# Kernel optimization log

Hardware: AMD Instinct MI355X
Metric: run time of the kernel (lower is better)

Reference implementation:

```python
import jax, jax.numpy as jnp
import numpy as np

ALPHA = 0.2  # LeakyReLU negative slope


def setup_inputs() -> dict:
    key = jax.random.key(0)
    k1, k2, k3, k4 = jax.random.split(key, 4)
    N, F_in, F_out = 8192, 512, 64
    x = jax.random.normal(k1, (N, F_in), dtype=jnp.float32)
    adj = jax.random.uniform(k2, (N, N), dtype=jnp.float32)
    W = jax.random.normal(k3, (F_in, F_out), dtype=jnp.float32) * 0.05
    a = jax.random.normal(k4, (2 * F_out, 1), dtype=jnp.float32) * 0.05
    return {"x": x, "adj": adj, "W": W, "a": a}


def reference(x, adj, W, a):
    F_out = W.shape[1]
    h = x @ W                                   # [N, F_out]
    # Additive attention decomposed: score[i,j] = h[i]·a1 + h[j]·a2
    # (equivalent to concat([h_i, h_j]) @ a, without the N×N×2F blowup)
    a1 = a[:F_out, 0]                           # [F_out]
    a2 = a[F_out:, 0]                           # [F_out]
    e = jax.nn.leaky_relu(h @ a1[:, None] + (h @ a2)[None, :], ALPHA)  # [N, N]
    attention = jax.nn.softmax(e * adj, axis=1)  # elementwise mult, as in source
    # dropout skipped (eval / training=False -> identity)
    h_prime = attention @ h                      # [N, F_out]
    return jax.nn.elu(h_prime)                   # concat=True branch
```

## Files before the change

kernel.cpp:

```cpp
#include <hip/hip_runtime.h>

#define ALPHA 0.2f

typedef __attribute__((ext_vector_type(2))) short short2v;
typedef __attribute__((ext_vector_type(8))) short short8v;
typedef __attribute__((ext_vector_type(4))) float f32x4;

__device__ __forceinline__ short f2bf(float f) {
  union { float f; unsigned u; } v; v.f = f;
  unsigned r = v.u + 0x7fffu + ((v.u >> 16) & 1u);
  return (short)(r >> 16);
}

__global__ __launch_bounds__(256) void k1_proj(
    const float* __restrict__ x, const float* __restrict__ W,
    const float* __restrict__ avec,
    short* __restrict__ hT, float* __restrict__ s1, float* __restrict__ s2) {
  __shared__ float xl[32 * 132];
  __shared__ float Wl[128 * 64];
  const int t   = threadIdx.x;
  const int rb  = blockIdx.x;
  const int row = t >> 3;
  const int fg  = t & 7;
  float acc[8];
#pragma unroll
  for (int e = 0; e < 8; e++) acc[e] = 0.f;

  for (int kc = 0; kc < 4; kc++) {
#pragma unroll
    for (int u = 0; u < 4; u++) {
      int lin = t + u * 256;
      int r = lin >> 5, c4 = lin & 31;
      float4 v = *(const float4*)(x + (size_t)(rb * 32 + r) * 512 + kc * 128 + c4 * 4);
      *(float4*)(xl + r * 132 + c4 * 4) = v;
    }
#pragma unroll
    for (int u = 0; u < 8; u++) {
      int lin = t + u * 256;
      int r = lin >> 4, c4 = lin & 15;
      float4 v = *(const float4*)(W + (size_t)(kc * 128 + r) * 64 + c4 * 4);
      *(float4*)(Wl + r * 64 + c4 * 4) = v;
    }
    __syncthreads();
#pragma unroll 8
    for (int k = 0; k < 128; k++) {
      float xv = xl[row * 132 + k];
      float4 w0 = *(const float4*)(Wl + k * 64 + fg * 8);
      float4 w1 = *(const float4*)(Wl + k * 64 + fg * 8 + 4);
      acc[0] = fmaf(xv, w0.x, acc[0]); acc[1] = fmaf(xv, w0.y, acc[1]);
      acc[2] = fmaf(xv, w0.z, acc[2]); acc[3] = fmaf(xv, w0.w, acc[3]);
      acc[4] = fmaf(xv, w1.x, acc[4]); acc[5] = fmaf(xv, w1.y, acc[5]);
      acc[6] = fmaf(xv, w1.z, acc[6]); acc[7] = fmaf(xv, w1.w, acc[7]);
    }
    __syncthreads();
  }

  float p1 = 0.f, p2 = 0.f;
#pragma unroll
  for (int e = 0; e < 8; e++) {
    p1 = fmaf(acc[e], avec[fg * 8 + e], p1);
    p2 = fmaf(acc[e], avec[64 + fg * 8 + e], p2);
  }
  p1 += __shfl_xor(p1, 1, 64); p1 += __shfl_xor(p1, 2, 64); p1 += __shfl_xor(p1, 4, 64);
  p2 += __shfl_xor(p2, 1, 64); p2 += __shfl_xor(p2, 2, 64); p2 += __shfl_xor(p2, 4, 64);
  const int gi = rb * 32 + row;
  if (fg == 0) { s1[gi] = p1; s2[gi] = p2; }
#pragma unroll
  for (int e = 0; e < 8; e++)
    hT[(size_t)(fg * 8 + e) * 8192 + gi] = f2bf(acc[e]);
}

__global__ __launch_bounds__(256, 2) void k2_attn(
    const float* __restrict__ adj, const short* __restrict__ hT,
    const float* __restrict__ s1, const float* __restrict__ s2,
    float* __restrict__ num, float* __restrict__ den) {
  __shared__ short hP[32768];
  __shared__ short Pl[8192];
  const int t    = threadIdx.x;
  const int wvi  = t >> 6;
  const int l    = t & 63;
  const int lq   = l >> 4;
  const int lr   = l & 15;
  const int rb   = blockIdx.x & 127;
  const int ks   = blockIdx.x >> 7;
  const int r0   = rb << 6;
  const int j0   = ks << 9;

#pragma unroll
  for (int r = 0; r < 16; r++) {
    const int d    = r * 4096 + t * 16;
    const int frow = d >> 10;
    const int lcb  = (d & 1023) ^ ((frow & 7) << 4);
    short8v v = *(const short8v*)(hT + (size_t)frow * 8192 + j0 + (lcb >> 1));
    *(short8v*)((char*)hP + d) = v;
  }
  __syncthreads();

  float s1r[16];
#pragma unroll
  for (int i = 0; i < 16; i++)
    s1r[i] = __int_as_float(
        __builtin_amdgcn_readfirstlane(__float_as_int(s1[r0 + wvi * 16 + i])));

  float denom_p[16];
#pragma unroll
  for (int i = 0; i < 16; i++) denom_p[i] = 0.f;

  f32x4 acc[4];
#pragma unroll
  for (int fb = 0; fb < 4; fb++) acc[fb] = (f32x4){0.f, 0.f, 0.f, 0.f};

  const float* arow0 = adj + (size_t)(r0 + wvi * 16) * 8192 + j0;
  const float* s2p   = s2 + j0;
  char* Pw = (char*)Pl + wvi * 4096;

  const int c0 = wvi & 3, c1 = (wvi + 1) & 3, c2 = (wvi + 2) & 3, c3 = (wvi + 3) & 3;

  float2 A0,A1,A2,A3,A4,A5,A6,A7,A8,A9,A10,A11,A12,A13,A14,A15;
  float2 B0,B1,B2,B3,B4,B5,B6,B7,B8,B9,B10,B11,B12,B13,B14,B15;
  float2 s2A, s2B;

#define LDADJ(S, CL) do { const float* ab__ = arow0 + (CL) * 128 + l * 2;     \
    S##0  = *(const float2*)(ab__);              S##1  = *(const float2*)(ab__ + 1 * 8192); \
    S##2  = *(const float2*)(ab__ + 2 * 8192);   S##3  = *(const float2*)(ab__ + 3 * 8192); \
    S##4  = *(const float2*)(ab__ + 4 * 8192);   S##5  = *(const float2*)(ab__ + 5 * 8192); \
    S##6  = *(const float2*)(ab__ + 6 * 8192);   S##7  = *(const float2*)(ab__ + 7 * 8192); \
    S##8  = *(const float2*)(ab__ + 8 * 8192);   S##9  = *(const float2*)(ab__ + 9 * 8192); \
    S##10 = *(const float2*)(ab__ + 10 * 8192);  S##11 = *(const float2*)(ab__ + 11 * 8192); \
    S##12 = *(const float2*)(ab__ + 12 * 8192);  S##13 = *(const float2*)(ab__ + 13 * 8192); \
    S##14 = *(const float2*)(ab__ + 14 * 8192);  S##15 = *(const float2*)(ab__ + 15 * 8192); \
  } while (0)

#define EXPROW(I, AV, S2V) do {                                               \
    float z0 = s1r[I] + S2V.x; z0 = fmaxf(z0, ALPHA * z0) * AV.x;             \
    float z1 = s1r[I] + S2V.y; z1 = fmaxf(z1, ALPHA * z1) * AV.y;             \
    float w0 = __expf(z0), w1 = __expf(z1);                                   \
    denom_p[I] += w0 + w1;                                                    \
    short2v pk = { f2bf(w0), f2bf(w1) };                                      \
    *(short2v*)(Pw + ((((I) << 8) + (l << 2)) ^ (((I) & 7) << 4))) = pk;      \
  } while (0)

#define K2_BODY(AS, S2, CL, PREF, CP) do {                                    \
    EXPROW(0, AS##0, S2);   EXPROW(1, AS##1, S2);   EXPROW(2, AS##2, S2);     \
    EXPROW(3, AS##3, S2);   EXPROW(4, AS##4, S2);   EXPROW(5, AS##5, S2);     \
    EXPROW(6, AS##6, S2);   EXPROW(7, AS##7, S2);   EXPROW(8, AS##8, S2);     \
    EXPROW(9, AS##9, S2);   EXPROW(10, AS##10, S2); EXPROW(11, AS##11, S2);   \
    EXPROW(12, AS##12, S2); EXPROW(13, AS##13, S2); EXPROW(14, AS##14, S2);   \
    EXPROW(15, AS##15, S2);                                                   \
    if (PREF) { LDADJ(AS, CP); S2 = *(const float2*)(s2p + (CP) * 128 + l * 2); } \
    _Pragma("unroll")                                                         \
    for (int kk = 0; kk < 4; kk++) {                                          \
      const int ab__ = ((lr << 8) + (kk << 6) + (lq << 4)) ^ ((lr & 7) << 4); \
      const short8v au = *(const short8v*)(Pw + ab__);                        \
      _Pragma("unroll")                                                       \
      for (int fb = 0; fb < 4; fb++) {                                        \
        const int fr__ = fb * 16 + lr;                                        \
        const int bb__ = ((fr__ << 10) + (((CL) << 8) + (kk << 6) + (lq << 4))) \
                         ^ ((fr__ & 7) << 4);                                 \
        const short8v bu = *(const short8v*)((char*)hP + bb__);               \
        acc[fb] = __builtin_amdgcn_mfma_f32_16x16x32_bf16(au, bu,             \
                                                          acc[fb], 0, 0, 0); \
      }                                                                       \
    }                                                                         \
  } while (0)

  LDADJ(A, c0); s2A = *(const float2*)(s2p + c0 * 128 + l * 2);
  LDADJ(B, c1); s2B = *(const float2*)(s2p + c1 * 128 + l * 2);

  K2_BODY(A, s2A, c0, 1, c2);
  K2_BODY(B, s2B, c1, 1, c3);
  K2_BODY(A, s2A, c2, 0, 0);
  K2_BODY(B, s2B, c3, 0, 0);
#undef LDADJ
#undef EXPROW
#undef K2_BODY

#pragma unroll
  for (int i = 0; i < 16; i++) {
    float d = denom_p[i];
    d += __shfl_xor(d, 1, 64); d += __shfl_xor(d, 2, 64);
    d += __shfl_xor(d, 4, 64); d += __shfl_xor(d, 8, 64);
    d += __shfl_xor(d, 16, 64); d += __shfl_xor(d, 32, 64);
    if (l == 0) den[(size_t)ks * 8192 + r0 + wvi * 16 + i] = d;
  }
  float* np = num + (size_t)ks * 524288;
#pragma unroll
  for (int fb = 0; fb < 4; fb++)
#pragma unroll
    for (int r = 0; r < 4; r++)
      np[(size_t)(r0 + wvi * 16 + lq * 4 + r) * 64 + fb * 16 + lr] = acc[fb][r];
}

__global__ __launch_bounds__(256) void k3_norm(
    const float* __restrict__ num, const float* __restrict__ den,
    float* __restrict__ out) {
  const int idx = blockIdx.x * 256 + threadIdx.x;
  const int row = idx >> 6;
  float n = 0.f, d = 0.f;
#pragma unroll
  for (int ksi = 0; ksi < 16; ksi++) {
    n += num[(size_t)ksi * 524288 + idx];
    d += den[ksi * 8192 + row];
  }
  float v = n / d;
  out[idx] = v > 0.f ? v : (__expf(v) - 1.f);
}

extern "C" void kernel_launch(void* const* d_in, const int* in_sizes, int n_in,
                              void* d_out, int out_size, void* d_ws, size_t ws_size,
                              hipStream_t stream) {
  const float* x   = (const float*)d_in[0];
  const float* adj = (const float*)d_in[1];
  const float* W   = (const float*)d_in[2];
  const float* av  = (const float*)d_in[3];
  float* out = (float*)d_out;
  char* ws = (char*)d_ws;

  short* hT  = (short*)ws;
  float* s1  = (float*)(ws + (1 << 20));
  float* s2  = (float*)(ws + (1 << 20) + 32768);
  float* num = (float*)(ws + (1 << 20) + 65536);
  float* den = num + 16u * 524288u;

  hipLaunchKernelGGL(k1_proj, dim3(256), dim3(256), 0, stream, x, W, av, hT, s1, s2);
  hipLaunchKernelGGL(k2_attn, dim3(2048), dim3(256), 0, stream,
                     adj, hT, s1, s2, num, den);
  hipLaunchKernelGGL(k3_norm, dim3(2048), dim3(256), 0, stream, num, den, out);
}
```

Baseline: 100.2 us.

## Front-load all adj loads as float4 and use packed bf16 conversion in attention kernel

Restructures the attention kernel so that every adjacency load for the 512-column slice is issued up front as float4, before the hT tile is written to LDS. This replaces the two-stage float2 prefetch pipeline. Each lane now computes four columns per row, converts with the hardware v_cvt_pk_bf16_f32 instruction, and writes P in two half-wave passes. It also replaces the readfirstlane s1 loads with shuffles and raises MFMA priority with s_setprio. The aim is more memory-level parallelism and fewer ALU instructions, at the cost of much higher register pressure (32 float4 plus 16 short8v live), which could reduce occupancy or cause spills.

Result: no change. 101.1 us (+0.9%).

```diff
diff --git a/kernel.cpp b/kernel.cpp
--- a/kernel.cpp
+++ b/kernel.cpp
@@ -2,14 +2,13 @@
 
 #define ALPHA 0.2f
 
-typedef __attribute__((ext_vector_type(2))) short short2v;
 typedef __attribute__((ext_vector_type(8))) short short8v;
 typedef __attribute__((ext_vector_type(4))) float f32x4;
 
-__device__ __forceinline__ short f2bf(float f) {
-  union { float f; unsigned u; } v; v.f = f;
-  unsigned r = v.u + 0x7fffu + ((v.u >> 16) & 1u);
-  return (short)(r >> 16);
+__device__ __forceinline__ unsigned cvt_pk_bf16(float a, float b) {
+  unsigned d;
+  asm("v_cvt_pk_bf16_f32 %0, %1, %2" : "=v"(d) : "v"(a), "v"(b));
+  return d;
 }
 
 __global__ __launch_bounds__(256) void k1_proj(
@@ -66,8 +65,11 @@
   const int gi = rb * 32 + row;
   if (fg == 0) { s1[gi] = p1; s2[gi] = p2; }
 #pragma unroll
-  for (int e = 0; e < 8; e++)
-    hT[(size_t)(fg * 8 + e) * 8192 + gi] = f2bf(acc[e]);
+  for (int e = 0; e < 8; e++) {
+    union { float f; unsigned u; } v; v.f = acc[e];
+    unsigned rr = v.u + 0x7fffu + ((v.u >> 16) & 1u);
+    hT[(size_t)(fg * 8 + e) * 8192 + gi] = (short)(rr >> 16);
+  }
 }
 
 __global__ __launch_bounds__(256, 2) void k2_attn(
@@ -86,94 +88,119 @@
   const int r0   = rb << 6;
   const int j0   = ks << 9;
 
+  float  s1own = s1[r0 + wvi * 16 + lr];
+  float4 s2A4  = *(const float4*)(s2 + j0 + l * 4);
+  float4 s2B4  = *(const float4*)(s2 + j0 + 256 + l * 4);
+
+  short8v sv[16];
 #pragma unroll
   for (int r = 0; r < 16; r++) {
     const int d    = r * 4096 + t * 16;
     const int frow = d >> 10;
     const int lcb  = (d & 1023) ^ ((frow & 7) << 4);
-    short8v v = *(const short8v*)(hT + (size_t)frow * 8192 + j0 + (lcb >> 1));
-    *(short8v*)((char*)hP + d) = v;
-  }
+    sv[r] = *(const short8v*)(hT + (size_t)frow * 8192 + j0 + (lcb >> 1));
+  }
+
+  const float* ar = adj + (size_t)(r0 + wvi * 16) * 8192 + j0 + l * 4;
+  float4 A0,A1,A2,A3,A4,A5,A6,A7,A8,A9,A10,A11,A12,A13,A14,A15;
+  float4 B0,B1,B2,B3,B4,B5,B6,B7,B8,B9,B10,B11,B12,B13,B14,B15;
+  A0  = *(const float4*)(ar);              B0  = *(const float4*)(ar + 256);
+  A1  = *(const float4*)(ar + 1 * 8192);   B1  = *(const float4*)(ar + 1 * 8192 + 256);
+  A2  = *(const float4*)(ar + 2 * 8192);   B2  = *(const float4*)(ar + 2 * 8192 + 256);
+  A3  = *(const float4*)(ar + 3 * 8192);   B3  = *(const float4*)(ar + 3 * 8192 + 256);
+  A4  = *(const float4*)(ar + 4 * 8192);   B4  = *(const float4*)(ar + 4 * 8192 + 256);
+  A5  = *(const float4*)(ar + 5 * 8192);   B5  = *(const float4*)(ar + 5 * 8192 + 256);
+  A6  = *(const float4*)(ar + 6 * 8192);   B6  = *(const float4*)(ar + 6 * 8192 + 256);
+  A7  = *(const float4*)(ar + 7 * 8192);   B7  = *(const float4*)(ar + 7 * 8192 + 256);
+  A8  = *(const float4*)(ar + 8 * 8192);   B8  = *(const float4*)(ar + 8 * 8192 + 256);
+  A9  = *(const float4*)(ar + 9 * 8192);   B9  = *(const float4*)(ar + 9 * 8192 + 256);
+  A10 = *(const float4*)(ar + 10 * 8192);  B10 = *(const float4*)(ar + 10 * 8192 + 256);
+  A11 = *(const float4*)(ar + 11 * 8192);  B11 = *(const float4*)(ar + 11 * 8192 + 256);
+  A12 = *(const float4*)(ar + 12 * 8192);  B12 = *(const float4*)(ar + 12 * 8192 + 256);
+  A13 = *(const float4*)(ar + 13 * 8192);  B13 = *(const float4*)(ar + 13 * 8192 + 256);
+  A14 = *(const float4*)(ar + 14 * 8192);  B14 = *(const float4*)(ar + 14 * 8192 + 256);
+  A15 = *(const float4*)(ar + 15 * 8192);  B15 = *(const float4*)(ar + 15 * 8192 + 256);
+
+#pragma unroll
+  for (int r = 0; r < 16; r++)
+    *(short8v*)((char*)hP + r * 4096 + t * 16) = sv[r];
   __syncthreads();
 
   float s1r[16];
 #pragma unroll
-  for (int i = 0; i < 16; i++)
-    s1r[i] = __int_as_float(
-        __builtin_amdgcn_readfirstlane(__float_as_int(s1[r0 + wvi * 16 + i])));
+  for (int i = 0; i < 16; i++) s1r[i] = __shfl(s1own, i, 64);
 
   float denom_p[16];
 #pragma unroll
   for (int i = 0; i < 16; i++) denom_p[i] = 0.f;
-
   f32x4 acc[4];
 #pragma unroll
   for (int fb = 0; fb < 4; fb++) acc[fb] = (f32x4){0.f, 0.f, 0.f, 0.f};
 
-  const float* arow0 = adj + (size_t)(r0 + wvi * 16) * 8192 + j0;
-  const float* s2p   = s2 + j0;
   char* Pw = (char*)Pl + wvi * 4096;
-
-  const int c0 = wvi & 3, c1 = (wvi + 1) & 3, c2 = (wvi + 2) & 3, c3 = (wvi + 3) & 3;
-
-  float2 A0,A1,A2,A3,A4,A5,A6,A7,A8,A9,A10,A11,A12,A13,A14,A15;
-  float2 B0,B1,B2,B3,B4,B5,B6,B7,B8,B9,B10,B11,B12,B13,B14,B15;
-  float2 s2A, s2B;
-
-#define LDADJ(S, CL) do { const float* ab__ = arow0 + (CL) * 128 + l * 2;     \
-    S##0  = *(const float2*)(ab__);              S##1  = *(const float2*)(ab__ + 1 * 8192); \
-    S##2  = *(const float2*)(ab__ + 2 * 8192);   S##3  = *(const float2*)(ab__ + 3 * 8192); \
-    S##4  = *(const float2*)(ab__ + 4 * 8192);   S##5  = *(const float2*)(ab__ + 5 * 8192); \
-    S##6  = *(const float2*)(ab__ + 6 * 8192);   S##7  = *(const float2*)(ab__ + 7 * 8192); \
-    S##8  = *(const float2*)(ab__ + 8 * 8192);   S##9  = *(const float2*)(ab__ + 9 * 8192); \
-    S##10 = *(const float2*)(ab__ + 10 * 8192);  S##11 = *(const float2*)(ab__ + 11 * 8192); \
-    S##12 = *(const float2*)(ab__ + 12 * 8192);  S##13 = *(const float2*)(ab__ + 13 * 8192); \
-    S##14 = *(const float2*)(ab__ + 14 * 8192);  S##15 = *(const float2*)(ab__ + 15 * 8192); \
-  } while (0)
-
-#define EXPROW(I, AV, S2V) do {                                               \
+  unsigned pk0[16], pk1[16];
+
+#define EXPROW4(I, AV, S2V) do {                                              \
     float z0 = s1r[I] + S2V.x; z0 = fmaxf(z0, ALPHA * z0) * AV.x;             \
     float z1 = s1r[I] + S2V.y; z1 = fmaxf(z1, ALPHA * z1) * AV.y;             \
-    float w0 = __expf(z0), w1 = __expf(z1);                                   \
-    denom_p[I] += w0 + w1;                                                    \
-    short2v pk = { f2bf(w0), f2bf(w1) };                                      \
-    *(short2v*)(Pw + ((((I) << 8) + (l << 2)) ^ (((I) & 7) << 4))) = pk;      \
+    float z2 = s1r[I] + S2V.z; z2 = fmaxf(z2, ALPHA * z2) * AV.z;             \
+    float z3 = s1r[I] + S2V.w; z3 = fmaxf(z3, ALPHA * z3) * AV.w;             \
+    float w0 = __expf(z0), w1 = __expf(z1), w2 = __expf(z2), w3 = __expf(z3); \
+    denom_p[I] += (w0 + w1) + (w2 + w3);                                      \
+    pk0[I] = cvt_pk_bf16(w0, w1); pk1[I] = cvt_pk_bf16(w2, w3);               \
   } while (0)
 
-#define K2_BODY(AS, S2, CL, PREF, CP) do {                                    \
-    EXPROW(0, AS##0, S2);   EXPROW(1, AS##1, S2);   EXPROW(2, AS##2, S2);     \
-    EXPROW(3, AS##3, S2);   EXPROW(4, AS##4, S2);   EXPROW(5, AS##5, S2);     \
-    EXPROW(6, AS##6, S2);   EXPROW(7, AS##7, S2);   EXPROW(8, AS##8, S2);     \
-    EXPROW(9, AS##9, S2);   EXPROW(10, AS##10, S2); EXPROW(11, AS##11, S2);   \
-    EXPROW(12, AS##12, S2); EXPROW(13, AS##13, S2); EXPROW(14, AS##14, S2);   \
-    EXPROW(15, AS##15, S2);                                                   \
-    if (PREF) { LDADJ(AS, CP); S2 = *(const float2*)(s2p + (CP) * 128 + l * 2); } \
+#define PWRITE(HALF) do {                                                     \
+    if ((l >> 5) == (HALF)) {                                                 \
+      const int cb = (l & 31) * 8;                                            \
+      _Pragma("unroll")                                                       \
+      for (int i2 = 0; i2 < 16; i2++) {                                       \
+        uint2 pv; pv.x = pk0[i2]; pv.y = pk1[i2];                             \
+        *(uint2*)(Pw + (((i2 << 8) + cb) ^ ((i2 & 7) << 4))) = pv;            \
+      }                                                                       \
+    }                                                                         \
+  } while (0)
+
+#define MFMACHUNK(CL) do {                                                    \
+    __builtin_amdgcn_s_setprio(1);                                            \
     _Pragma("unroll")                                                         \
     for (int kk = 0; kk < 4; kk++) {                                          \
-      const int ab__ = ((lr << 8) + (kk << 6) + (lq << 4)) ^ ((lr & 7) << 4); \
-      const short8v au = *(const short8v*)(Pw + ab__);                        \
+      const int ab = ((lr << 8) + (kk << 6) + (lq << 4)) ^ ((lr & 7) << 4);   \
+      const short8v au = *(const short8v*)(Pw + ab);                          \
       _Pragma("unroll")                                                       \
       for (int fb = 0; fb < 4; fb++) {                                        \
-        const int fr__ = fb * 16 + lr;                                        \
-        const int bb__ = ((fr__ << 10) + (((CL) << 8) + (kk << 6) + (lq << 4))) \
-                         ^ ((fr__ & 7) << 4);                                 \
-        const short8v bu = *(const short8v*)((char*)hP + bb__);               \
+        const int fr = fb * 16 + lr;                                          \
+        const int bb = ((fr << 10) + ((CL) << 8) + (kk << 6) + (lq << 4))     \
+                       ^ ((fr & 7) << 4);                                     \
+        const short8v bu = *(const short8v*)((char*)hP + bb);                 \
         acc[fb] = __builtin_amdgcn_mfma_f32_16x16x32_bf16(au, bu,             \
                                                           acc[fb], 0, 0, 0); \
       }                                                                       \
     }                                                                         \
+    __builtin_amdgcn_s_setprio(0);                                            \
   } while (0)
 
-  LDADJ(A, c0); s2A = *(const float2*)(s2p + c0 * 128 + l * 2);
-  LDADJ(B, c1); s2B = *(const float2*)(s2p + c1 * 128 + l * 2);
-
-  K2_BODY(A, s2A, c0, 1, c2);
-  K2_BODY(B, s2B, c1, 1, c3);
-  K2_BODY(A, s2A, c2, 0, 0);
-  K2_BODY(B, s2B, c3, 0, 0);
-#undef LDADJ
-#undef EXPROW
-#undef K2_BODY
+  EXPROW4(0, A0, s2A4);   EXPROW4(1, A1, s2A4);   EXPROW4(2, A2, s2A4);
+  EXPROW4(3, A3, s2A4);   EXPROW4(4, A4, s2A4);   EXPROW4(5, A5, s2A4);
+  EXPROW4(6, A6, s2A4);   EXPROW4(7, A7, s2A4);   EXPROW4(8, A8, s2A4);
+  EXPROW4(9, A9, s2A4);   EXPROW4(10, A10, s2A4); EXPROW4(11, A11, s2A4);
+  EXPROW4(12, A12, s2A4); EXPROW4(13, A13, s2A4); EXPROW4(14, A14, s2A4);
+  EXPROW4(15, A15, s2A4);
+  PWRITE(0); MFMACHUNK(0);
+  PWRITE(1); MFMACHUNK(1);
+
+  EXPROW4(0, B0, s2B4);   EXPROW4(1, B1, s2B4);   EXPROW4(2, B2, s2B4);
+  EXPROW4(3, B3, s2B4);   EXPROW4(4, B4, s2B4);   EXPROW4(5, B5, s2B4);
+  EXPROW4(6, B6, s2B4);   EXPROW4(7, B7, s2B4);   EXPROW4(8, B8, s2B4);
+  EXPROW4(9, B9, s2B4);   EXPROW4(10, B10, s2B4); EXPROW4(11, B11, s2B4);
+  EXPROW4(12, B12, s2B4); EXPROW4(13, B13, s2B4); EXPROW4(14, B14, s2B4);
+  EXPROW4(15, B15, s2B4);
+  PWRITE(0); MFMACHUNK(2);
+  PWRITE(1); MFMACHUNK(3);
+
+#undef EXPROW4
+#undef PWRITE
+#undef MFMACHUNK
 
 #pragma unroll
   for (int i = 0; i < 16; i++) {
```
